# Performance work log

Measured on AMD Instinct MI355X. Metric: run time of the kernel, lower is better.

Reference implementation:

```python
import jax, jax.numpy as jnp
import numpy as np

TOL = 5
SEG_PENALTY = 2.0
SEG_REWARD = 1.0
PROX_REWARD = 2.0
FAR_PENALTY = 1.5
CLASS_WEIGHTS = np.array([0.1, 0.1, 5.0, 5.0], dtype=np.float32)


def setup_inputs() -> dict:
    key = jax.random.key(0)
    k1, k2, k3 = jax.random.split(key, 3)
    B, S, C = 128, 32768, 4
    logits = jax.random.normal(k1, (B, S, C), dtype=jnp.float32)
    labels = jax.random.randint(k2, (B, S), 0, 4, dtype=jnp.int32)
    seg_marks = jax.random.randint(k3, (B, S), 0, 2, dtype=jnp.int32)
    return {"logits": logits, "labels": labels, "seg_marks": seg_marks}


def _window_any(x_bool, tol):
    # sliding 'any' over a symmetric window of size 2*tol+1 along the seq axis
    xi = x_bool.astype(jnp.int32)
    w = jax.lax.reduce_window(xi, 0, jax.lax.max, (1, 2 * tol + 1), (1, 1), 'SAME')
    return w > 0


def reference(logits, labels, seg_marks):
    B, S, C = logits.shape
    weights = jnp.asarray(CLASS_WEIGHTS)

    # weighted cross-entropy, reduction='none', ignore_index=-100
    ignored = labels == -100
    safe_labels = jnp.where(ignored, 0, labels)
    logz = jax.nn.logsumexp(logits, axis=-1)                       # [B,S]
    picked = jnp.take_along_axis(logits, safe_labels[..., None], axis=-1)[..., 0]
    base_loss = weights[safe_labels] * (logz - picked)
    base_loss = jnp.where(ignored, 0.0, base_loss)

    predictions = jnp.argmax(logits, axis=-1)
    pred_sw = predictions >= 2                                      # [B,S]
    true_sw = labels >= 2                                           # [B,S]

    adj = jnp.zeros_like(base_loss)

    # segmentation alignment: gated by pred_sw
    seg_pos = seg_marks > 0
    zcol = jnp.zeros((B, 1), dtype=bool)
    seg_prev1 = jnp.concatenate([zcol, seg_pos[:, :-1]], axis=1)    # seg[t-1]>0
    seg_prev2 = jnp.concatenate([zcol, zcol, seg_pos[:, :-2]], axis=1)
    seg_next1 = jnp.concatenate([seg_pos[:, 1:], zcol], axis=1)     # seg[t+1]>0
    penalty_cond = seg_prev1 | seg_prev2                            # break => add once
    reward_cond = seg_pos | seg_next1                               # if/elif => once
    adj = adj + pred_sw * (SEG_PENALTY * penalty_cond.astype(jnp.float32)
                           - SEG_REWARD * reward_cond.astype(jnp.float32))

    # proximity reward: true switch with any predicted switch within +/- TOL
    pred_near = _window_any(pred_sw, TOL)
    adj = adj - PROX_REWARD * (true_sw & pred_near).astype(jnp.float32)

    # far penalty: predicted switch with no true switch within +/- TOL
    # (only applies when the row has at least one true switch)
    true_near = _window_any(true_sw, TOL)
    has_true = jnp.any(true_sw, axis=1, keepdims=True)
    adj = adj + FAR_PENALTY * (pred_sw & has_true & (~true_near)).astype(jnp.float32)

    adjusted = base_loss + adj
    valid = (labels != -100).astype(jnp.float32)
    return (adjusted * valid).sum() / valid.sum()
```

## Files before the change

### kernel.cpp

```cpp
#include <hip/hip_runtime.h>


typedef unsigned long long u64;

#define PPT 8
#define POSW (64 * PPT)
#define NT 256
#define WPB (NT / 64)

#if __has_builtin(__builtin_amdgcn_exp2f)
#define EXP2F(x) __builtin_amdgcn_exp2f(x)
#else
#define EXP2F(x) exp2f(x)
#endif
#if __has_builtin(__builtin_amdgcn_logf)
#define LOG2F(x) __builtin_amdgcn_logf(x)
#else
#define LOG2F(x) log2f(x)
#endif

__device__ __forceinline__ u64 smearw(u64 lo, u64 hi) {
#pragma unroll
    for (int s = 0; s < 4; ++s) {
        const int k = (s == 0) ? 1 : (s == 1) ? 2 : (s == 2) ? 4 : 3;
        const u64 nhi = hi | (hi << k) | (lo >> (64 - k));
        lo = lo | (lo << k);
        hi = nhi;
    }
    return (lo >> 10) | (hi << 54);
}

static __global__ __launch_bounds__(NT) void
loss_kernel(const float4* __restrict__ logits, const int* __restrict__ labels,
            const int* __restrict__ seg, uint2* __restrict__ parts) {
    const int S = 32768;
    const int t = threadIdx.x;
    const int w = t >> 6, lane = t & 63;
    const int gw = blockIdx.x * WPB + w;
    const int wpr = S / POSW;
    const int b = gw >> 6;
    const int span = (gw & (wpr - 1)) * POSW;

    const size_t rowoff = (size_t)b * S;
    const float4* lrow = logits + rowoff;
    const int* labrow = labels + rowoff;
    const int* segrow = seg + rowoff;

    const int p0 = span + lane;
    float4 g[PPT];
    int lab[PPT], sg[PPT];
#pragma unroll
    for (int j = 0; j < PPT; ++j) g[j] = lrow[p0 + j * 64];
#pragma unroll
    for (int j = 0; j < PPT; ++j) lab[j] = labrow[p0 + j * 64];
#pragma unroll
    for (int j = 0; j < PPT; ++j) sg[j] = segrow[p0 + j * 64];

    const bool fl = lane < 5;
    const bool use = (lane < 10) && (fl ? (span > 0) : (span + POSW < S));
    const int fpos = fl ? (span - 5 + lane) : (span + POSW + lane - 5);
    float4 fg = make_float4(0.f, 0.f, 0.f, 0.f);
    int flb = 0, fsg = 0;
    if (use) { fg = lrow[fpos]; flb = labrow[fpos]; fsg = segrow[fpos]; }
    const u64 fbp = __ballot(use && (fmaxf(fg.z, fg.w) > fmaxf(fg.x, fg.y)));
    const u64 fbt = __ballot(use && (flb >= 2));
    const u64 fbs = __ballot(use && (fsg > 0));
    const u64 l5p = fbp & 31u, r5p = (fbp >> 5) & 31u;
    const u64 l5t = fbt & 31u, r5t = (fbt >> 5) & 31u;
    const u64 l5s = fbs & 31u, r5s = (fbs >> 5) & 31u;

    const float L2E = 1.4426950408889634f;
    const float LN2 = 0.69314718055994531f;
    u64 pm[PPT], tm[PPT], sm[PPT];
    float ce = 0.0f;
#pragma unroll
    for (int j = 0; j < PPT; ++j) {
        const float mab = fmaxf(g[j].x, g[j].y), mcd = fmaxf(g[j].z, g[j].w);
        pm[j] = __ballot(mcd > mab);
        tm[j] = __ballot(lab[j] >= 2);
        sm[j] = __ballot(sg[j] > 0);
        const float se = EXP2F(g[j].x * L2E) + EXP2F(g[j].y * L2E) +
                         EXP2F(g[j].z * L2E) + EXP2F(g[j].w * L2E);
        const float picked = (lab[j] < 2) ? (lab[j] == 0 ? g[j].x : g[j].y)
                                          : (lab[j] == 2 ? g[j].z : g[j].w);
        const float wt = (lab[j] >= 2) ? 5.0f : 0.1f;
        ce += wt * (LN2 * LOG2F(se) - picked);
    }

    int npc = 0, nrc = 0, npr = 0, nfar = 0;
#pragma unroll
    for (int j = 0; j < PPT; ++j) {
        const u64 pp5 = j ? (pm[j - 1] >> 59) : l5p;
        const u64 pn5 = (j < PPT - 1) ? (pm[j + 1] & 31u) : r5p;
        const u64 tp5 = j ? (tm[j - 1] >> 59) : l5t;
        const u64 tn5 = (j < PPT - 1) ? (tm[j + 1] & 31u) : r5t;
        const u64 sp5 = j ? (sm[j - 1] >> 59) : l5s;
        const u64 sn5 = (j < PPT - 1) ? (sm[j + 1] & 31u) : r5s;

        const u64 pn = smearw((pm[j] << 5) | pp5, (pm[j] >> 59) | (pn5 << 5));
        const u64 tn = smearw((tm[j] << 5) | tp5, (tm[j] >> 59) | (tn5 << 5));
        const u64 slo = (sm[j] << 5) | sp5;
        const u64 shi = (sm[j] >> 59) | (sn5 << 5);
        const u64 pc = ((slo >> 3) | (shi << 61)) | ((slo >> 4) | (shi << 60));
        const u64 rc = ((slo >> 5) | (shi << 59)) | ((slo >> 6) | (shi << 58));

        npc += __popcll(pm[j] & pc);
        nrc += __popcll(pm[j] & rc);
        npr += __popcll(tm[j] & pn);
        nfar += __popcll(pm[j] & ~tn);
    }
    const u64 anyt = tm[0] | tm[1] | tm[2] | tm[3] | tm[4] | tm[5] | tm[6] | tm[7];

#pragma unroll
    for (int off = 32; off > 0; off >>= 1) ce += __shfl_down(ce, off);
    if (lane == 0) {
        const float tot = ce + (float)(2 * npc - nrc - 2 * npr);
        const unsigned pk = (unsigned)nfar | ((anyt ? 1u : 0u) << 12);
        parts[gw] = make_uint2(__float_as_uint(tot), pk);
    }
}

static __global__ __launch_bounds__(1024) void
finalize_kernel(const uint2* __restrict__ parts, float* __restrict__ out) {
    const int t = threadIdx.x;
    __shared__ int s_far[128], s_hta[128];
    __shared__ double s_ds[16];
    __shared__ int s_ff[16];
    if (t < 128) { s_far[t] = 0; s_hta[t] = 0; }
    __syncthreads();

    double ds = 0.0;
#pragma unroll
    for (int k = 0; k < 8; ++k) {
        const int i = t + k * 1024;
        const uint2 p = parts[i];
        ds += (double)__uint_as_float(p.x);
        const int nf = (int)(p.y & 4095u);
        const int row = i >> 6;
        if (nf) atomicAdd(&s_far[row], nf);
        if (p.y & (1u << 12)) s_hta[row] = 1;
    }
#pragma unroll
    for (int off = 32; off > 0; off >>= 1) ds += __shfl_down(ds, off);
    if ((t & 63) == 0) s_ds[t >> 6] = ds;
    __syncthreads();

    int f = (t < 128 && s_hta[t]) ? s_far[t] : 0;
#pragma unroll
    for (int off = 32; off > 0; off >>= 1) f += __shfl_down(f, off);
    if ((t & 63) == 0) s_ff[t >> 6] = f;
    __syncthreads();

    if (t == 0) {
        double Ssum = 0.0;
        int F = 0;
#pragma unroll
        for (int i = 0; i < 16; ++i) { Ssum += s_ds[i]; F += s_ff[i]; }
        out[0] = (float)((Ssum + 1.5 * (double)F) / 4194304.0);
    }
}

extern "C" void kernel_launch(void* const* d_in, const int* in_sizes, int n_in,
                              void* d_out, int out_size, void* d_ws, size_t ws_size,
                              hipStream_t stream) {
    const float4* logits = (const float4*)d_in[0];
    const int* labels = (const int*)d_in[1];
    const int* seg = (const int*)d_in[2];
    float* out = (float*)d_out;

    const int B = 128;
    const int S = 32768;
    const int grid = B * (S / (POSW * WPB));

    uint2* parts = (uint2*)d_ws;

    loss_kernel<<<grid, NT, 0, stream>>>(logits, labels, seg, parts);
    finalize_kernel<<<1, 1024, 0, stream>>>(parts, out);
}
```

Before: 29.09 us.

## Fuse finalize into loss kernel via last-block atomic counter reduction

Drops the separate finalize kernel launch. Each block increments a global counter, and the last block to finish does the cross-block reduction, with the counter reset by a memset before launch. Block size doubles to 512 and the grid halves. The bitmask window logic becomes a rolling streaming form that keeps fewer live u64 masks and splits the CE accumulation by class weight. This trades one kernel launch for a memset node plus fences and a serial tail in the last block.

New measurement: 62.36 us. +114.3%, slower.

```diff
diff --git a/kernel.cpp b/kernel.cpp
--- a/kernel.cpp
+++ b/kernel.cpp
@@ -5,8 +5,10 @@
 
 #define PPT 8
 #define POSW (64 * PPT)
-#define NT 256
+#define NT 512
 #define WPB (NT / 64)
+#define GRID 1024
+#define NPARTS 8192
 
 #if __has_builtin(__builtin_amdgcn_exp2f)
 #define EXP2F(x) __builtin_amdgcn_exp2f(x)
@@ -30,16 +32,37 @@
     return (lo >> 10) | (hi << 54);
 }
 
+__device__ __forceinline__ void winmath(u64 pm, u64 tm, u64 sm,
+                                        u64 pp5, u64 tp5, u64 sp5,
+                                        u64 pn5, u64 tn5, u64 sn5,
+                                        int& npc, int& nrc, int& npr, int& nfar) {
+    const u64 pn = smearw((pm << 5) | pp5, (pm >> 59) | (pn5 << 5));
+    const u64 tn = smearw((tm << 5) | tp5, (tm >> 59) | (tn5 << 5));
+    const u64 slo = (sm << 5) | sp5;
+    const u64 shi = (sm >> 59) | (sn5 << 5);
+    const u64 pc = ((slo >> 3) | (shi << 61)) | ((slo >> 4) | (shi << 60));
+    const u64 rc = ((slo >> 5) | (shi << 59)) | ((slo >> 6) | (shi << 58));
+    npc += __popcll(pm & pc);
+    nrc += __popcll(pm & rc);
+    npr += __popcll(tm & pn);
+    nfar += __popcll(pm & ~tn);
+}
+
 static __global__ __launch_bounds__(NT) void
-loss_kernel(const float4* __restrict__ logits, const int* __restrict__ labels,
-            const int* __restrict__ seg, uint2* __restrict__ parts) {
+loss_fused(const float4* __restrict__ logits, const int* __restrict__ labels,
+           const int* __restrict__ seg, u64* __restrict__ parts,
+           int* __restrict__ cnt, float* __restrict__ out) {
     const int S = 32768;
     const int t = threadIdx.x;
     const int w = t >> 6, lane = t & 63;
     const int gw = blockIdx.x * WPB + w;
-    const int wpr = S / POSW;
     const int b = gw >> 6;
-    const int span = (gw & (wpr - 1)) * POSW;
+    const int span = (gw & 63) * POSW;
+
+    __shared__ int s_last;
+    __shared__ int s_far[128], s_hta[128];
+    __shared__ double s_ds[WPB];
+    __shared__ int s_fw[WPB];
 
     const size_t rowoff = (size_t)b * S;
     const float4* lrow = logits + rowoff;
@@ -65,98 +88,91 @@
     const u64 fbp = __ballot(use && (fmaxf(fg.z, fg.w) > fmaxf(fg.x, fg.y)));
     const u64 fbt = __ballot(use && (flb >= 2));
     const u64 fbs = __ballot(use && (fsg > 0));
-    const u64 l5p = fbp & 31u, r5p = (fbp >> 5) & 31u;
-    const u64 l5t = fbt & 31u, r5t = (fbt >> 5) & 31u;
-    const u64 l5s = fbs & 31u, r5s = (fbs >> 5) & 31u;
+    const u64 r5p = (fbp >> 5) & 31u, r5t = (fbt >> 5) & 31u, r5s = (fbs >> 5) & 31u;
 
     const float L2E = 1.4426950408889634f;
     const float LN2 = 0.69314718055994531f;
-    u64 pm[PPT], tm[PPT], sm[PPT];
-    float ce = 0.0f;
+    u64 pmA = 0, tmA = 0, smA = 0;
+    u64 pt5 = fbp & 31u, tt5 = fbt & 31u, st5 = fbs & 31u;
+    int npc = 0, nrc = 0, npr = 0, nfar = 0;
+    u64 anyt = 0;
+    float ce_lo = 0.0f, ce_hi = 0.0f;
 #pragma unroll
     for (int j = 0; j < PPT; ++j) {
-        const float mab = fmaxf(g[j].x, g[j].y), mcd = fmaxf(g[j].z, g[j].w);
-        pm[j] = __ballot(mcd > mab);
-        tm[j] = __ballot(lab[j] >= 2);
-        sm[j] = __ballot(sg[j] > 0);
-        const float se = EXP2F(g[j].x * L2E) + EXP2F(g[j].y * L2E) +
-                         EXP2F(g[j].z * L2E) + EXP2F(g[j].w * L2E);
-        const float picked = (lab[j] < 2) ? (lab[j] == 0 ? g[j].x : g[j].y)
-                                          : (lab[j] == 2 ? g[j].z : g[j].w);
-        const float wt = (lab[j] >= 2) ? 5.0f : 0.1f;
-        ce += wt * (LN2 * LOG2F(se) - picked);
+        const float4 gj = g[j];
+        const float mab = fmaxf(gj.x, gj.y), mcd = fmaxf(gj.z, gj.w);
+        const u64 pmB = __ballot(mcd > mab);
+        const u64 tmB = __ballot(lab[j] >= 2);
+        const u64 smB = __ballot(sg[j] > 0);
+        anyt |= tmB;
+
+        const float se = EXP2F(gj.x * L2E) + EXP2F(gj.y * L2E) +
+                         EXP2F(gj.z * L2E) + EXP2F(gj.w * L2E);
+        const float p01 = (lab[j] == 0) ? gj.x : gj.y;
+        const float p23 = (lab[j] == 2) ? gj.z : gj.w;
+        const float picked = (lab[j] < 2) ? p01 : p23;
+        const float d = LN2 * LOG2F(se) - picked;
+        ce_hi += (lab[j] >= 2) ? d : 0.0f;
+        ce_lo += (lab[j] >= 2) ? 0.0f : d;
+
+        if (j > 0) {
+            winmath(pmA, tmA, smA, pt5, tt5, st5,
+                    pmB & 31u, tmB & 31u, smB & 31u, npc, nrc, npr, nfar);
+            pt5 = pmA >> 59; tt5 = tmA >> 59; st5 = smA >> 59;
+        }
+        pmA = pmB; tmA = tmB; smA = smB;
     }
+    winmath(pmA, tmA, smA, pt5, tt5, st5, r5p, r5t, r5s, npc, nrc, npr, nfar);
 
-    int npc = 0, nrc = 0, npr = 0, nfar = 0;
-#pragma unroll
-    for (int j = 0; j < PPT; ++j) {
-        const u64 pp5 = j ? (pm[j - 1] >> 59) : l5p;
-        const u64 pn5 = (j < PPT - 1) ? (pm[j + 1] & 31u) : r5p;
-        const u64 tp5 = j ? (tm[j - 1] >> 59) : l5t;
-        const u64 tn5 = (j < PPT - 1) ? (tm[j + 1] & 31u) : r5t;
-        const u64 sp5 = j ? (sm[j - 1] >> 59) : l5s;
-        const u64 sn5 = (j < PPT - 1) ? (sm[j + 1] & 31u) : r5s;
-
-        const u64 pn = smearw((pm[j] << 5) | pp5, (pm[j] >> 59) | (pn5 << 5));
-        const u64 tn = smearw((tm[j] << 5) | tp5, (tm[j] >> 59) | (tn5 << 5));
-        const u64 slo = (sm[j] << 5) | sp5;
-        const u64 shi = (sm[j] >> 59) | (sn5 << 5);
-        const u64 pc = ((slo >> 3) | (shi << 61)) | ((slo >> 4) | (shi << 60));
-        const u64 rc = ((slo >> 5) | (shi << 59)) | ((slo >> 6) | (shi << 58));
-
-        npc += __popcll(pm[j] & pc);
-        nrc += __popcll(pm[j] & rc);
-        npr += __popcll(tm[j] & pn);
-        nfar += __popcll(pm[j] & ~tn);
-    }
-    const u64 anyt = tm[0] | tm[1] | tm[2] | tm[3] | tm[4] | tm[5] | tm[6] | tm[7];
-
+    float ce = 5.0f * ce_hi + 0.1f * ce_lo;
 #pragma unroll
     for (int off = 32; off > 0; off >>= 1) ce += __shfl_down(ce, off);
     if (lane == 0) {
         const float tot = ce + (float)(2 * npc - nrc - 2 * npr);
         const unsigned pk = (unsigned)nfar | ((anyt ? 1u : 0u) << 12);
-        parts[gw] = make_uint2(__float_as_uint(tot), pk);
+        parts[gw] = ((u64)pk << 32) | (u64)__float_as_uint(tot);
     }
-}
 
-static __global__ __launch_bounds__(1024) void
-finalize_kernel(const uint2* __restrict__ parts, float* __restrict__ out) {
-    const int t = threadIdx.x;
-    __shared__ int s_far[128], s_hta[128];
-    __shared__ double s_ds[16];
-    __shared__ int s_ff[16];
+    __syncthreads();
+    if (t == 0) {
+        __threadfence();
+        s_last = (atomicAdd(cnt, 1) == GRID - 1);
+    }
+    __syncthreads();
+    if (!s_last) return;
+    __threadfence();
+
     if (t < 128) { s_far[t] = 0; s_hta[t] = 0; }
     __syncthreads();
 
     double ds = 0.0;
 #pragma unroll
-    for (int k = 0; k < 8; ++k) {
-        const int i = t + k * 1024;
-        const uint2 p = parts[i];
-        ds += (double)__uint_as_float(p.x);
-        const int nf = (int)(p.y & 4095u);
+    for (int k = 0; k < NPARTS / NT; ++k) {
+        const int i = t + k * NT;
+        const u64 p = parts[i];
+        ds += (double)__uint_as_float((unsigned)p);
+        const unsigned pk = (unsigned)(p >> 32);
+        const int nf = (int)(pk & 0xFFFu);
         const int row = i >> 6;
         if (nf) atomicAdd(&s_far[row], nf);
-        if (p.y & (1u << 12)) s_hta[row] = 1;
+        if (pk & (1u << 12)) s_hta[row] = 1;
     }
+    __syncthreads();
+
+    int fv = (t < 128 && s_hta[t]) ? s_far[t] : 0;
+#pragma unroll
+    for (int off = 32; off > 0; off >>= 1) fv += __shfl_down(fv, off);
 #pragma unroll
     for (int off = 32; off > 0; off >>= 1) ds += __shfl_down(ds, off);
-    if ((t & 63) == 0) s_ds[t >> 6] = ds;
-    __syncthreads();
-
-    int f = (t < 128 && s_hta[t]) ? s_far[t] : 0;
-#pragma unroll
-    for (int off = 32; off > 0; off >>= 1) f += __shfl_down(f, off);
-    if ((t & 63) == 0) s_ff[t >> 6] = f;
+    if (lane == 0) { s_ds[w] = ds; s_fw[w] = fv; }
     __syncthreads();
 
     if (t == 0) {
-        double Ssum = 0.0;
+        double Ss = 0.0;
         int F = 0;
 #pragma unroll
-        for (int i = 0; i < 16; ++i) { Ssum += s_ds[i]; F += s_ff[i]; }
-        out[0] = (float)((Ssum + 1.5 * (double)F) / 4194304.0);
+        for (int i = 0; i < WPB; ++i) { Ss += s_ds[i]; F += s_fw[i]; }
+        out[0] = (float)((Ss + 1.5 * (double)F) / 4194304.0);
     }
 }
 
@@ -168,12 +184,9 @@
     const int* seg = (const int*)d_in[2];
     float* out = (float*)d_out;
 
-    const int B = 128;
-    const int S = 32768;
-    const int grid = B * (S / (POSW * WPB));
+    u64* parts = (u64*)d_ws;
+    int* cnt = (int*)((char*)d_ws + NPARTS * 8);
 
-    uint2* parts = (uint2*)d_ws;
-
-    loss_kernel<<<grid, NT, 0, stream>>>(logits, labels, seg, parts);
-    finalize_kernel<<<1, 1024, 0, stream>>>(parts, out);
+    hipMemsetAsync(cnt, 0, 4, stream);
+    loss_fused<<<GRID, NT, 0, stream>>>(logits, labels, seg, parts, cnt, out);
 }
```
